# Kernel tuning notes

Measured on AMD Instinct MI355X. Metric: run time of the kernel, lower is better.

The kernel has to match this reference:

```python
import jax, jax.numpy as jnp
import numpy as np

HEADS = 4
OUT_DIM = 64
NEG_SLOPE = 0.2


def setup_inputs() -> dict:
    key = jax.random.key(0)
    k1, k2, k3, k4 = jax.random.split(key, 4)
    n, in_dim = 4096, 256
    x = jax.random.normal(k1, (n, in_dim), dtype=jnp.float32)
    adj = jax.random.randint(k2, (n, n), 0, 2, dtype=jnp.int32)
    # lin: in_dim -> heads*out_dim (no bias), stored as [in_dim, heads*out_dim]
    W = jax.random.normal(k3, (in_dim, HEADS * OUT_DIM), dtype=jnp.float32) * 0.05
    # att_weight: [heads, 2*out_dim]
    att = jax.random.normal(k4, (HEADS, 2 * OUT_DIM), dtype=jnp.float32) * 0.05
    return {"x": x, "adj": adj, "W": W, "att": att}


def reference(x, adj, W, att):
    n = x.shape[0]
    h = (x @ W).reshape(n, HEADS, OUT_DIM)  # [n, H, D]
    # scores[i,j,h] = att[h] . cat(h_i, h_j) = <h_i, a_src[h]> + <h_j, a_dst[h]>
    a_src, a_dst = att[:, :OUT_DIM], att[:, OUT_DIM:]
    e_src = jnp.einsum('nhd,hd->nh', h, a_src)  # [n, H]
    e_dst = jnp.einsum('nhd,hd->nh', h, a_dst)  # [n, H]
    scores = e_src[:, None, :] + e_dst[None, :, :]  # [n, n, H]
    scores = jax.nn.leaky_relu(scores, negative_slope=NEG_SLOPE)
    mask = (adj > 0)[:, :, None]  # [n, n, 1]
    scores = jnp.where(mask, scores, -jnp.inf)
    alpha = jax.nn.softmax(scores, axis=1)  # softmax over neighbors j
    # h_prime[i,h,d] = sum_j alpha[i,j,h] * h[j,h,d]
    h_prime = jnp.einsum('ijh,jhd->ihd', alpha, h)
    return h_prime.reshape(n, HEADS * OUT_DIM)
```

## Files before the change

### kernel.cpp

```cpp
#include <hip/hip_runtime.h>
#include <hip/hip_bf16.h>

#define HEADS 4
#define ODIM 64
#define HD 256
#define NEG_SLOPE 0.2f
#define SPLITS 4

typedef __attribute__((ext_vector_type(8))) short bf16x8;
typedef __attribute__((ext_vector_type(4))) float floatx4;
typedef __attribute__((ext_vector_type(2))) float floatx2;

__global__ __launch_bounds__(256) void pack_xw(const float* __restrict__ x,
                                               const float* __restrict__ W,
                                               __hip_bfloat16* __restrict__ xh,
                                               __hip_bfloat16* __restrict__ xl,
                                               __hip_bfloat16* __restrict__ wh,
                                               __hip_bfloat16* __restrict__ wl,
                                               int K, int nxb) {
    const int b = blockIdx.x;
    const int Kc = K >> 5;
    if (b < nxb) {
        const int g = b * 256 + threadIdx.x;
        const int lane = g & 63, frag = g >> 6;
        const int kc = frag % Kc, mc = frag / Kc;
        const int l16 = lane & 15, q = lane >> 4;
        const float* src = x + (size_t)(mc * 16 + l16) * K + kc * 32 + q * 8;
        const float4 v0 = *(const float4*)src;
        const float4 v1 = *(const float4*)(src + 4);
        const float vv[8] = {v0.x, v0.y, v0.z, v0.w, v1.x, v1.y, v1.z, v1.w};
        union { __hip_bfloat16 b[8]; bf16x8 v; } H, L;
        #pragma unroll
        for (int p = 0; p < 8; ++p) {
            H.b[p] = __float2bfloat16(vv[p]);
            L.b[p] = __float2bfloat16(vv[p] - __bfloat162float(H.b[p]));
        }
        *(bf16x8*)&xh[(size_t)frag * 512 + lane * 8] = H.v;
        *(bf16x8*)&xl[(size_t)frag * 512 + lane * 8] = L.v;
    } else {
        const int g = (b - nxb) * 256 + threadIdx.x;
        const int lane = g & 63, frag = g >> 6;
        const int kc = frag % Kc, nc = frag / Kc;
        const int l16 = lane & 15, q = lane >> 4;
        union { __hip_bfloat16 b[8]; bf16x8 v; } H, L;
        #pragma unroll
        for (int p = 0; p < 8; ++p) {
            const float w = W[(size_t)(kc * 32 + q * 8 + p) * HD + nc * 16 + l16];
            H.b[p] = __float2bfloat16(w);
            L.b[p] = __float2bfloat16(w - __bfloat162float(H.b[p]));
        }
        *(bf16x8*)&wh[(size_t)frag * 512 + lane * 8] = H.v;
        *(bf16x8*)&wl[(size_t)frag * 512 + lane * 8] = L.v;
    }
}

__global__ __launch_bounds__(256) void compress_adj(const int* __restrict__ adj,
                                                    unsigned int* __restrict__ bits, int n) {
    const int wid = (blockIdx.x * 256 + threadIdx.x) >> 6;
    const int lane = threadIdx.x & 63;
    const int nq = n >> 10;
    const int i = wid / nq;
    const int jb = (wid % nq) << 10;
    const int nw = n >> 5;
    #pragma unroll 4
    for (int jj = 0; jj < 16; ++jj) {
        const int j = jb + jj * 64 + lane;
        const unsigned long long m = __ballot(adj[(size_t)i * n + j] > 0);
        if (lane == 0) {
            uint2 u;
            u.x = (unsigned int)m;
            u.y = (unsigned int)(m >> 32);
            *(uint2*)&bits[(size_t)i * nw + ((jb + jj * 64) >> 5)] = u;
        }
    }
}

__global__ __launch_bounds__(128) void gemm_fused(
    const __hip_bfloat16* __restrict__ xh, const __hip_bfloat16* __restrict__ xl,
    const __hip_bfloat16* __restrict__ wh, const __hip_bfloat16* __restrict__ wl,
    const float* __restrict__ att, float2* __restrict__ esrc, float2* __restrict__ edst,
    __hip_bfloat16* __restrict__ hbB, int n, int K) {

    __shared__ __hip_bfloat16 T[64][40];

    const int tid = threadIdx.x, wave = tid >> 6, lane = tid & 63;
    const int q = lane >> 4, l16 = lane & 15;
    const int m0 = blockIdx.x * 32;
    const int head = blockIdx.y;
    const int Kc = K >> 5;
    const int mc = (m0 >> 4) + wave;

    floatx4 acc[4] = {{0.f,0.f,0.f,0.f},{0.f,0.f,0.f,0.f},{0.f,0.f,0.f,0.f},{0.f,0.f,0.f,0.f}};

    const __hip_bfloat16* Axh = xh + (size_t)mc * Kc * 512 + lane * 8;
    const __hip_bfloat16* Axl = xl + (size_t)mc * Kc * 512 + lane * 8;
    const __hip_bfloat16* Bwh = wh + lane * 8;
    const __hip_bfloat16* Bwl = wl + lane * 8;
    #pragma unroll 2
    for (int kc = 0; kc < Kc; ++kc) {
        const bf16x8 ah = *(const bf16x8*)(Axh + (size_t)kc * 512);
        const bf16x8 al = *(const bf16x8*)(Axl + (size_t)kc * 512);
        bf16x8 bh[4], bl[4];
        #pragma unroll
        for (int nt = 0; nt < 4; ++nt) {
            const size_t fo = (size_t)((head * 4 + nt) * Kc + kc) * 512;
            bh[nt] = *(const bf16x8*)(Bwh + fo);
            bl[nt] = *(const bf16x8*)(Bwl + fo);
        }
        #pragma unroll
        for (int nt = 0; nt < 4; ++nt)
            acc[nt] = __builtin_amdgcn_mfma_f32_16x16x32_bf16(ah, bh[nt], acc[nt], 0, 0, 0);
        #pragma unroll
        for (int nt = 0; nt < 4; ++nt)
            acc[nt] = __builtin_amdgcn_mfma_f32_16x16x32_bf16(ah, bl[nt], acc[nt], 0, 0, 0);
        #pragma unroll
        for (int nt = 0; nt < 4; ++nt)
            acc[nt] = __builtin_amdgcn_mfma_f32_16x16x32_bf16(al, bh[nt], acc[nt], 0, 0, 0);
    }

    float as_v[4], ad_v[4];
    #pragma unroll
    for (int nt = 0; nt < 4; ++nt) {
        as_v[nt] = att[head * 2 * ODIM + nt * 16 + l16];
        ad_v[nt] = att[head * 2 * ODIM + ODIM + nt * 16 + l16];
    }
    #pragma unroll
    for (int r = 0; r < 4; ++r) {
        float ps = 0.f, pd = 0.f;
        #pragma unroll
        for (int nt = 0; nt < 4; ++nt) {
            ps = fmaf(acc[nt][r], as_v[nt], ps);
            pd = fmaf(acc[nt][r], ad_v[nt], pd);
        }
        #pragma unroll
        for (int m = 1; m <= 8; m <<= 1) {
            ps += __shfl_xor(ps, m, 64);
            pd += __shfl_xor(pd, m, 64);
        }
        if (l16 == 0) {
            const int i = m0 + wave * 16 + q * 4 + r;
            esrc[head * n + i] = make_float2(__expf(ps), __expf(NEG_SLOPE * ps));
            edst[head * n + i] = make_float2(__expf(pd), __expf(NEG_SLOPE * pd));
        }
    }

    #pragma unroll
    for (int nt = 0; nt < 4; ++nt) {
        union { __hip_bfloat16 b[4]; uint2 u; } pk;
        #pragma unroll
        for (int r = 0; r < 4; ++r) pk.b[r] = __float2bfloat16(acc[nt][r]);
        *(uint2*)&T[nt * 16 + l16][wave * 16 + q * 4] = pk.u;
    }
    __syncthreads();

    #pragma unroll
    for (int ffi = 0; ffi < 2; ++ffi) {
        const int f = wave + ffi * 2;
        const bf16x8 v = *(const bf16x8*)&T[f * 16 + l16][q * 8];
        const size_t frag = ((size_t)head * (n >> 5) + (m0 >> 5)) * 4 + f;
        *(bf16x8*)&hbB[frag * 512 + lane * 8] = v;
    }
}

__global__ __launch_bounds__(256, 2) void aggregate(
    const unsigned int* __restrict__ bits, const float2* __restrict__ esrc,
    const float2* __restrict__ edst, const __hip_bfloat16* __restrict__ hbB,
    float* __restrict__ outsp, float* __restrict__ densp, int n, int KR) {

    const int tid = threadIdx.x;
    const int wave = tid >> 6, lane = tid & 63;
    const int q = lane >> 4, l16 = lane & 15;
    const int i0 = blockIdx.x * 32;
    const int K0 = blockIdx.y * KR;
    const int nw = n >> 5;

    floatx2 es12[2];
    #pragma unroll
    for (int mt = 0; mt < 2; ++mt) {
        const float2 e = esrc[wave * n + i0 + mt * 16 + l16];
        es12[mt][0] = e.x; es12[mt][1] = e.y;
    }

    union { short s[8]; bf16x8 v; } bones;
    #pragma unroll
    for (int p = 0; p < 8; ++p) bones.s[p] = (l16 == 0) ? (short)0x3F80 : (short)0;

    floatx4 acc[2][4];
    floatx4 accd[2];
    #pragma unroll
    for (int mt = 0; mt < 2; ++mt) {
        accd[mt] = (floatx4){0.f, 0.f, 0.f, 0.f};
        #pragma unroll
        for (int nt = 0; nt < 4; ++nt) acc[mt][nt] = (floatx4){0.f, 0.f, 0.f, 0.f};
    }

    const unsigned int* brow0 = bits + (size_t)(i0 + l16) * nw + (K0 >> 5);
    const unsigned int* brow1 = bits + (size_t)(i0 + 16 + l16) * nw + (K0 >> 5);
    const float2* edp = edst + (size_t)wave * n + K0 + q * 8;
    const __hip_bfloat16* hb = hbB + ((size_t)wave * (n >> 5) + (K0 >> 5)) * 4 * 512 + lane * 8;

    const int NSTEP = KR >> 5;

    unsigned int cw0, cw1; float4 ced[4]; bf16x8 cbf[4];
    cw0 = brow0[0]; cw1 = brow1[0];
    {
        const float4* ep = (const float4*)edp;
        ced[0] = ep[0]; ced[1] = ep[1]; ced[2] = ep[2]; ced[3] = ep[3];
        #pragma unroll
        for (int nt = 0; nt < 4; ++nt)
            cbf[nt] = *(const bf16x8*)&hb[(size_t)nt * 512];
    }

    for (int s = 0; s < NSTEP; ++s) {
        unsigned int nw0, nw1; float4 ned[4]; bf16x8 nbf[4];
        const int sn = (s + 1 < NSTEP) ? s + 1 : s;
        nw0 = brow0[sn]; nw1 = brow1[sn];
        {
            const float4* ep = (const float4*)(edp + (size_t)sn * 32);
            ned[0] = ep[0]; ned[1] = ep[1]; ned[2] = ep[2]; ned[3] = ep[3];
            #pragma unroll
            for (int nt = 0; nt < 4; ++nt)
                nbf[nt] = *(const bf16x8*)&hb[((size_t)sn * 4 + nt) * 512];
        }

        #pragma unroll
        for (int mt = 0; mt < 2; ++mt) {
            const unsigned int bm = ((mt ? cw1 : cw0) >> (q * 8)) & 0xFFu;
            union { unsigned int u[4]; bf16x8 v; } af;
            #pragma unroll
            for (int p = 0; p < 4; ++p) {
                const float4 e = ced[p];
                floatx2 e0; e0[0] = e.x; e0[1] = e.y;
                floatx2 e1; e1[0] = e.z; e1[1] = e.w;
                const floatx2 pa = es12[mt] * e0;
                const floatx2 pb = es12[mt] * e1;
                const float wa = fmaxf(pa[0], pa[1]);
                const float wb = fmaxf(pb[0], pb[1]);
                const unsigned int b2 = (bm >> (2 * p)) & 3u;
                const unsigned int mm = (b2 & 1u) * 0xFFFFu | (b2 >> 1) * 0xFFFF0000u;
                af.u[p] = __builtin_amdgcn_perm(__float_as_uint(wb), __float_as_uint(wa),
                                                0x07060302u) & mm;
            }
            #pragma unroll
            for (int nt = 0; nt < 4; ++nt)
                acc[mt][nt] = __builtin_amdgcn_mfma_f32_16x16x32_bf16(af.v, cbf[nt], acc[mt][nt], 0, 0, 0);
            accd[mt] = __builtin_amdgcn_mfma_f32_16x16x32_bf16(af.v, bones.v, accd[mt], 0, 0, 0);
        }

        cw0 = nw0; cw1 = nw1;
        #pragma unroll
        for (int p = 0; p < 4; ++p) ced[p] = ned[p];
        #pragma unroll
        for (int nt = 0; nt < 4; ++nt) cbf[nt] = nbf[nt];
    }

    const size_t sOut = (size_t)blockIdx.y * n * HD;
    #pragma unroll
    for (int mt = 0; mt < 2; ++mt)
        #pragma unroll
        for (int nt = 0; nt < 4; ++nt)
            #pragma unroll
            for (int r = 0; r < 4; ++r)
                outsp[sOut + (size_t)(i0 + mt * 16 + q * 4 + r) * HD + wave * ODIM + nt * 16 + l16] = acc[mt][nt][r];
    if (l16 == 0) {
        #pragma unroll
        for (int mt = 0; mt < 2; ++mt)
            #pragma unroll
            for (int r = 0; r < 4; ++r)
                densp[((size_t)blockIdx.y * n + i0 + mt * 16 + q * 4 + r) * HEADS + wave] = accd[mt][r];
    }
}

__global__ __launch_bounds__(256) void normalize(const float* __restrict__ outsp,
                                                 const float* __restrict__ densp,
                                                 float* __restrict__ out, int n, int splits) {
    const int g = blockIdx.x * 256 + threadIdx.x;
    const int i = g >> 6;
    const int c4 = (g & 63) * 4;
    const int head = c4 >> 6;
    float den = 0.f;
    for (int s = 0; s < splits; ++s) den += densp[((size_t)s * n + i) * HEADS + head];
    float4 v = {0.f, 0.f, 0.f, 0.f};
    for (int s = 0; s < splits; ++s) {
        const float4 t = *(const float4*)&outsp[(size_t)s * n * HD + (size_t)i * HD + c4];
        v.x += t.x; v.y += t.y; v.z += t.z; v.w += t.w;
    }
    const float inv = 1.0f / den;
    v.x *= inv; v.y *= inv; v.z *= inv; v.w *= inv;
    *(float4*)&out[(size_t)i * HD + c4] = v;
}

extern "C" void kernel_launch(void* const* d_in, const int* in_sizes, int n_in,
                              void* d_out, int out_size, void* d_ws, size_t ws_size,
                              hipStream_t stream) {
    const float* x   = (const float*)d_in[0];
    const int*   adj = (const int*)d_in[1];
    const float* W   = (const float*)d_in[2];
    const float* att = (const float*)d_in[3];
    float* out = (float*)d_out;

    const int in_dim = in_sizes[2] / HD;
    const int n = in_sizes[0] / in_dim;

    char* ws = (char*)d_ws;
    size_t off = 0;
    auto alloc = [&](size_t bytes) -> void* {
        void* p = ws + off; off += (bytes + 255) & ~(size_t)255; return p;
    };
    __hip_bfloat16* xh = (__hip_bfloat16*)alloc((size_t)n * in_dim * 2);
    __hip_bfloat16* xl = (__hip_bfloat16*)alloc((size_t)n * in_dim * 2);
    __hip_bfloat16* wh = (__hip_bfloat16*)alloc((size_t)in_dim * HD * 2);
    __hip_bfloat16* wl = (__hip_bfloat16*)alloc((size_t)in_dim * HD * 2);
    float2* esrc = (float2*)alloc((size_t)HEADS * n * 8);
    float2* edst = (float2*)alloc((size_t)HEADS * n * 8);
    __hip_bfloat16* hbB = (__hip_bfloat16*)alloc((size_t)n * HD * 2);
    unsigned int* bits = (unsigned int*)alloc((size_t)n * (n / 8));

    const size_t outB = (size_t)n * HD * 4, denB = (size_t)n * HEADS * 4;
    float* densp = (float*)alloc((size_t)SPLITS * denB);
    float* outsp = (float*)alloc((size_t)SPLITS * outB);

    const int nxb = (n / 16) * (in_dim / 32) * 64 / 256;
    const int nwb = (HD / 16) * (in_dim / 32) * 64 / 256;
    pack_xw<<<nxb + nwb, 256, 0, stream>>>(x, W, xh, xl, wh, wl, in_dim, nxb);
    compress_adj<<<(n * (n >> 10)) / 4, 256, 0, stream>>>(adj, bits, n);
    gemm_fused<<<dim3(n / 32, HEADS), 128, 0, stream>>>(xh, xl, wh, wl, att, esrc, edst, hbB, n, in_dim);
    aggregate<<<dim3(n / 32, SPLITS), 256, 0, stream>>>(bits, esrc, edst, hbB, outsp, densp, n, n / SPLITS);
    normalize<<<n * 64 / 256, 256, 0, stream>>>(outsp, densp, out, n, SPLITS);
}
```

Before: 166.9 us.

## Fuse adjacency compression into aggregate, read int32 adj directly, raise splits

Removes the separate compress_adj kernel and its bitmask buffer. The aggregate kernel now loads the int32 adjacency rows itself and masks the attention weights with per-element compares. It also moves the edst and hb prefetch to adj-only prefetch, asks for 4 blocks per CU in launch bounds, and uses 8 K-splits when workspace allows. This saves one launch and a bitmask write and re-read. In exchange, each aggregate block reads 32x more adjacency bytes, since adj is no longer shared through a compact bitmask, and partial-sum traffic grows with more splits.

```diff
diff --git a/kernel.cpp b/kernel.cpp
--- a/kernel.cpp
+++ b/kernel.cpp
@@ -5,7 +5,6 @@
 #define ODIM 64
 #define HD 256
 #define NEG_SLOPE 0.2f
-#define SPLITS 4
 
 typedef __attribute__((ext_vector_type(8))) short bf16x8;
 typedef __attribute__((ext_vector_type(4))) float floatx4;
@@ -54,27 +53,6 @@
     }
 }
 
-__global__ __launch_bounds__(256) void compress_adj(const int* __restrict__ adj,
-                                                    unsigned int* __restrict__ bits, int n) {
-    const int wid = (blockIdx.x * 256 + threadIdx.x) >> 6;
-    const int lane = threadIdx.x & 63;
-    const int nq = n >> 10;
-    const int i = wid / nq;
-    const int jb = (wid % nq) << 10;
-    const int nw = n >> 5;
-    #pragma unroll 4
-    for (int jj = 0; jj < 16; ++jj) {
-        const int j = jb + jj * 64 + lane;
-        const unsigned long long m = __ballot(adj[(size_t)i * n + j] > 0);
-        if (lane == 0) {
-            uint2 u;
-            u.x = (unsigned int)m;
-            u.y = (unsigned int)(m >> 32);
-            *(uint2*)&bits[(size_t)i * nw + ((jb + jj * 64) >> 5)] = u;
-        }
-    }
-}
-
 __global__ __launch_bounds__(128) void gemm_fused(
     const __hip_bfloat16* __restrict__ xh, const __hip_bfloat16* __restrict__ xl,
     const __hip_bfloat16* __restrict__ wh, const __hip_bfloat16* __restrict__ wl,
@@ -162,8 +140,8 @@
     }
 }
 
-__global__ __launch_bounds__(256, 2) void aggregate(
-    const unsigned int* __restrict__ bits, const float2* __restrict__ esrc,
+__global__ __launch_bounds__(256, 4) void aggregate(
+    const int* __restrict__ adj, const float2* __restrict__ esrc,
     const float2* __restrict__ edst, const __hip_bfloat16* __restrict__ hbB,
     float* __restrict__ outsp, float* __restrict__ densp, int n, int KR) {
 
@@ -172,7 +150,6 @@
     const int q = lane >> 4, l16 = lane & 15;
     const int i0 = blockIdx.x * 32;
     const int K0 = blockIdx.y * KR;
-    const int nw = n >> 5;
 
     floatx2 es12[2];
     #pragma unroll
@@ -194,38 +171,33 @@
         for (int nt = 0; nt < 4; ++nt) acc[mt][nt] = (floatx4){0.f, 0.f, 0.f, 0.f};
     }
 
-    const unsigned int* brow0 = bits + (size_t)(i0 + l16) * nw + (K0 >> 5);
-    const unsigned int* brow1 = bits + (size_t)(i0 + 16 + l16) * nw + (K0 >> 5);
+    const int* arow0 = adj + (size_t)(i0 + l16) * n + K0 + q * 8;
+    const int* arow1 = arow0 + (size_t)16 * n;
     const float2* edp = edst + (size_t)wave * n + K0 + q * 8;
     const __hip_bfloat16* hb = hbB + ((size_t)wave * (n >> 5) + (K0 >> 5)) * 4 * 512 + lane * 8;
 
     const int NSTEP = KR >> 5;
 
-    unsigned int cw0, cw1; float4 ced[4]; bf16x8 cbf[4];
-    cw0 = brow0[0]; cw1 = brow1[0];
+    int4 aj[4];
     {
-        const float4* ep = (const float4*)edp;
-        ced[0] = ep[0]; ced[1] = ep[1]; ced[2] = ep[2]; ced[3] = ep[3];
-        #pragma unroll
-        for (int nt = 0; nt < 4; ++nt)
-            cbf[nt] = *(const bf16x8*)&hb[(size_t)nt * 512];
+        const int4* p0 = (const int4*)arow0;
+        const int4* p1 = (const int4*)arow1;
+        aj[0] = p0[0]; aj[1] = p0[1]; aj[2] = p1[0]; aj[3] = p1[1];
     }
 
     for (int s = 0; s < NSTEP; ++s) {
-        unsigned int nw0, nw1; float4 ned[4]; bf16x8 nbf[4];
-        const int sn = (s + 1 < NSTEP) ? s + 1 : s;
-        nw0 = brow0[sn]; nw1 = brow1[sn];
+        float4 ced[4]; bf16x8 cbf[4];
         {
-            const float4* ep = (const float4*)(edp + (size_t)sn * 32);
-            ned[0] = ep[0]; ned[1] = ep[1]; ned[2] = ep[2]; ned[3] = ep[3];
+            const float4* ep = (const float4*)(edp + (size_t)s * 32);
+            ced[0] = ep[0]; ced[1] = ep[1]; ced[2] = ep[2]; ced[3] = ep[3];
             #pragma unroll
             for (int nt = 0; nt < 4; ++nt)
-                nbf[nt] = *(const bf16x8*)&hb[((size_t)sn * 4 + nt) * 512];
-        }
-
+                cbf[nt] = *(const bf16x8*)&hb[((size_t)s * 4 + nt) * 512];
+        }
+
+        const int* av = (const int*)aj;
         #pragma unroll
         for (int mt = 0; mt < 2; ++mt) {
-            const unsigned int bm = ((mt ? cw1 : cw0) >> (q * 8)) & 0xFFu;
             union { unsigned int u[4]; bf16x8 v; } af;
             #pragma unroll
             for (int p = 0; p < 4; ++p) {
@@ -234,12 +206,12 @@
                 floatx2 e1; e1[0] = e.z; e1[1] = e.w;
                 const floatx2 pa = es12[mt] * e0;
                 const floatx2 pb = es12[mt] * e1;
-                const float wa = fmaxf(pa[0], pa[1]);
-                const float wb = fmaxf(pb[0], pb[1]);
-                const unsigned int b2 = (bm >> (2 * p)) & 3u;
-                const unsigned int mm = (b2 & 1u) * 0xFFFFu | (b2 >> 1) * 0xFFFF0000u;
+                float wa = fmaxf(pa[0], pa[1]);
+                float wb = fmaxf(pb[0], pb[1]);
+                wa = (av[mt * 8 + 2 * p]     > 0) ? wa : 0.0f;
+                wb = (av[mt * 8 + 2 * p + 1] > 0) ? wb : 0.0f;
                 af.u[p] = __builtin_amdgcn_perm(__float_as_uint(wb), __float_as_uint(wa),
-                                                0x07060302u) & mm;
+                                                0x07060302u);
             }
             #pragma unroll
             for (int nt = 0; nt < 4; ++nt)
@@ -247,11 +219,12 @@
             accd[mt] = __builtin_amdgcn_mfma_f32_16x16x32_bf16(af.v, bones.v, accd[mt], 0, 0, 0);
         }
 
-        cw0 = nw0; cw1 = nw1;
-        #pragma unroll
-        for (int p = 0; p < 4; ++p) ced[p] = ned[p];
-        #pragma unroll
-        for (int nt = 0; nt < 4; ++nt) cbf[nt] = nbf[nt];
+        const int sn = (s + 1 < NSTEP) ? s + 1 : s;
+        {
+            const int4* p0 = (const int4*)(arow0 + (size_t)sn * 32);
+            const int4* p1 = (const int4*)(arow1 + (size_t)sn * 32);
+            aj[0] = p0[0]; aj[1] = p0[1]; aj[2] = p1[0]; aj[3] = p1[1];
+        }
     }
 
     const size_t sOut = (size_t)blockIdx.y * n * HD;
@@ -314,17 +287,16 @@
     float2* esrc = (float2*)alloc((size_t)HEADS * n * 8);
     float2* edst = (float2*)alloc((size_t)HEADS * n * 8);
     __hip_bfloat16* hbB = (__hip_bfloat16*)alloc((size_t)n * HD * 2);
-    unsigned int* bits = (unsigned int*)alloc((size_t)n * (n / 8));
 
     const size_t outB = (size_t)n * HD * 4, denB = (size_t)n * HEADS * 4;
-    float* densp = (float*)alloc((size_t)SPLITS * denB);
-    float* outsp = (float*)alloc((size_t)SPLITS * outB);
+    int splits = (ws_size >= off + 8 * (outB + denB)) ? 8 : 4;
+    float* densp = (float*)alloc((size_t)splits * denB);
+    float* outsp = (float*)alloc((size_t)splits * outB);
 
     const int nxb = (n / 16) * (in_dim / 32) * 64 / 256;
     const int nwb = (HD / 16) * (in_dim / 32) * 64 / 256;
     pack_xw<<<nxb + nwb, 256, 0, stream>>>(x, W, xh, xl, wh, wl, in_dim, nxb);
-    compress_adj<<<(n * (n >> 10)) / 4, 256, 0, stream>>>(adj, bits, n);
     gemm_fused<<<dim3(n / 32, HEADS), 128, 0, stream>>>(xh, xl, wh, wl, att, esrc, edst, hbB, n, in_dim);
-    aggregate<<<dim3(n / 32, SPLITS), 256, 0, stream>>>(bits, esrc, edst, hbB, outsp, densp, n, n / SPLITS);
-    normalize<<<n * 64 / 256, 256, 0, stream>>>(outsp, densp, out, n, SPLITS);
-}
+    aggregate<<<dim3(n / 32, splits), 256, 0, stream>>>(adj, esrc, edst, hbB, outsp, densp, n, n / splits);
+    normalize<<<n * 64 / 256, 256, 0, stream>>>(outsp, densp, out, n, splits);
+}
```

Result: no change. 168.2 us (+0.7%).
